# Optimization experiments

Hardware: AMD Instinct MI355X
Metric: run time of the kernel (lower is better)

Reference implementation:

```python
import jax, jax.numpy as jnp
import numpy as np

N_HEADS = 16
D_MODEL = 1024
D_K = D_MODEL // N_HEADS
B, S = 2, 2048


def setup_inputs() -> dict:
    key = jax.random.key(0)
    ks = jax.random.split(key, 12)
    sc = 1.0 / np.sqrt(D_MODEL)
    inp = {
        'query': jax.random.normal(ks[0], (B, S, D_MODEL), jnp.float32),
        'key':   jax.random.normal(ks[1], (B, S, D_MODEL), jnp.float32),
        'value': jax.random.normal(ks[2], (B, S, D_MODEL), jnp.float32),
        'mask':  jnp.ones((B, 1, 1, S), jnp.int32),
        'Wq': jax.random.normal(ks[3], (D_MODEL, D_MODEL), jnp.float32) * sc,
        'bq': jnp.zeros((D_MODEL,), jnp.float32),
        'Wk': jax.random.normal(ks[4], (D_MODEL, D_MODEL), jnp.float32) * sc,
        'bk': jnp.zeros((D_MODEL,), jnp.float32),
        'Wv': jax.random.normal(ks[5], (D_MODEL, D_MODEL), jnp.float32) * sc,
        'bv': jnp.zeros((D_MODEL,), jnp.float32),
        'Wo': jax.random.normal(ks[6], (D_MODEL, D_MODEL), jnp.float32) * sc,
        'bo': jnp.zeros((D_MODEL,), jnp.float32),
    }
    return inp


def reference(query, key, value, mask, Wq, bq, Wk, bk, Wv, bv, Wo, bo):
    # Linear projections (torch Linear: x @ W.T + b)
    q = query @ Wq.T + bq
    k = key @ Wk.T + bk
    v = value @ Wv.T + bv
    # [B, S, D] -> [B, H, S, d_k]
    def split_heads(x):
        b, s, _ = x.shape
        return x.reshape(b, s, N_HEADS, D_K).transpose(0, 2, 1, 3)
    q, k, v = split_heads(q), split_heads(k), split_heads(v)
    # scaled dot-product attention with explicit [B,H,S,S] scores
    att = jnp.einsum('bhqd,bhkd->bhqk', q, k) / jnp.sqrt(jnp.float32(D_K))
    att = jnp.where(mask == 0, -jnp.inf, att)
    scores = jax.nn.softmax(att, axis=-1)
    # dropout is identity in eval/reference mode
    out = jnp.einsum('bhqk,bhkd->bhqd', scores, v)
    b = out.shape[0]
    out = out.transpose(0, 2, 1, 3).reshape(b, -1, N_HEADS * D_K)
    return out @ Wo.T + bo
```

## Files before the change

kernel.cpp:

```cpp
#include <hip/hip_runtime.h>
#include <hip/hip_bf16.h>

#define DM   1024
#define SLEN 2048
#define NH   16
#define DK   64

typedef float f32x4 __attribute__((ext_vector_type(4)));
typedef short short8 __attribute__((ext_vector_type(8)));
typedef short short4v __attribute__((ext_vector_type(4)));

__device__ __forceinline__ unsigned short f2bf(float f) {
  union { float f; unsigned int u; } x; x.f = f;
  unsigned int r = x.u + 0x7fffu + ((x.u >> 16) & 1u);
  return (unsigned short)(r >> 16);
}

__device__ __forceinline__ void gload_lds16(const unsigned short* g, unsigned short* l) {
  __builtin_amdgcn_global_load_lds(
      (const __attribute__((address_space(1))) unsigned int*)g,
      (__attribute__((address_space(3))) unsigned int*)l, 16, 0, 0);
}

__device__ __forceinline__ f32x4 mfma32(short8 a, short8 b, f32x4 c) {
  return __builtin_amdgcn_mfma_f32_16x16x32_bf16(a, b, c, 0, 0, 0);
}

__device__ __forceinline__ f32x4 mfma16(short4v a, short4v b, f32x4 c) {
#if __has_builtin(__builtin_amdgcn_mfma_f32_16x16x16bf16_1k)
  return __builtin_amdgcn_mfma_f32_16x16x16bf16_1k(a, b, c, 0, 0, 0);
#else
  f32x4 d;
  asm volatile("v_mfma_f32_16x16x16_bf16 %0, %1, %2, %3"
               : "=v"(d) : "v"(a), "v"(b), "v"(c));
  return d;
#endif
}

struct ConvArgs { const float* src[7]; unsigned short* dst[7]; };

__global__ __launch_bounds__(256) void conv_kernel(ConvArgs a) {
  int blk = blockIdx.x, seg, base;
  if (blk < 6144) { seg = blk >> 11; base = blk & 2047; }
  else { int t = blk - 6144; seg = 3 + (t >> 9); base = t & 511; }
  const float* s = a.src[seg];
  unsigned short* d = a.dst[seg];
  int idx = (base * 256 + (int)threadIdx.x) * 8;
  float4 v0 = *(const float4*)(s + idx);
  float4 v1 = *(const float4*)(s + idx + 4);
  unsigned short o[8];
  o[0]=f2bf(v0.x); o[1]=f2bf(v0.y); o[2]=f2bf(v0.z); o[3]=f2bf(v0.w);
  o[4]=f2bf(v1.x); o[5]=f2bf(v1.y); o[6]=f2bf(v1.z); o[7]=f2bf(v1.w);
  *(uint4*)(d + idx) = *(uint4*)o;
}

template <int TN>
__device__ __forceinline__ void gemm_core(int mode,
                                          const unsigned short* __restrict__ A,
                                          const unsigned short* __restrict__ W,
                                          const float* __restrict__ bias,
                                          void* __restrict__ outp, float scale,
                                          int m0, int n0,
                                          unsigned short* As, unsigned short* Bs) {
  const int tid = threadIdx.x;
  const int lane = tid & 63;
  const int l15 = lane & 15;
  const int quad = lane >> 4;
  const int wv = tid >> 6;
  const int wm = (wv >> 1) * 64, wn = (wv & 1) * (TN / 2);
  const int NB = TN / 32;

  f32x4 acc[4][NB];
#pragma unroll
  for (int i = 0; i < 4; ++i)
#pragma unroll
    for (int j = 0; j < NB; ++j) acc[i][j] = (f32x4){0.f, 0.f, 0.f, 0.f};

  for (int k0 = 0; k0 < DM; k0 += 64) {
    __syncthreads();
#pragma unroll
    for (int i = 0; i < 4; ++i) {
      int c = tid + i * 256;
      int row = c >> 3, sc = ((c & 7) ^ (row & 7)) << 3;
      gload_lds16(A + (size_t)(m0 + row) * DM + k0 + sc, As + c * 8);
    }
#pragma unroll
    for (int i = 0; i < NB; ++i) {
      int c = tid + i * 256;
      int row = c >> 3, sc = ((c & 7) ^ (row & 7)) << 3;
      gload_lds16(W + (size_t)(n0 + row) * DM + k0 + sc, Bs + c * 8);
    }
    __syncthreads();
    short8 af[4][2], bf[NB][2];
#pragma unroll
    for (int i = 0; i < 4; ++i) {
      int r = wm + i * 16 + l15;
#pragma unroll
      for (int kf = 0; kf < 2; ++kf)
        af[i][kf] = *(const short8*)(As + r * 64 + (((kf * 4 + quad) ^ (r & 7)) << 3));
    }
#pragma unroll
    for (int j = 0; j < NB; ++j) {
      int r = wn + j * 16 + l15;
#pragma unroll
      for (int kf = 0; kf < 2; ++kf)
        bf[j][kf] = *(const short8*)(Bs + r * 64 + (((kf * 4 + quad) ^ (r & 7)) << 3));
    }
#pragma unroll
    for (int kf = 0; kf < 2; ++kf)
#pragma unroll
      for (int i = 0; i < 4; ++i)
#pragma unroll
        for (int j = 0; j < NB; ++j)
          acc[i][j] = mfma32(af[i][kf], bf[j][kf], acc[i][j]);
  }

#pragma unroll
  for (int i = 0; i < 4; ++i)
#pragma unroll
    for (int j = 0; j < NB; ++j) {
      int col = n0 + wn + j * 16 + l15;
      float bv = bias[col];
      int row0 = wm + i * 16 + (quad << 2) + m0;
      if (mode == 2) {
        unsigned short pk[4];
#pragma unroll
        for (int g = 0; g < 4; ++g) pk[g] = f2bf(acc[i][j][g] + bv);
        int d = col & (DK - 1), hh = col >> 6;
        int brow = row0 >> 11, srow = row0 & (SLEN - 1);
        size_t idx = ((size_t)((brow * NH + hh) * DK + d)) * SLEN + srow;
        *(uint2*)(((unsigned short*)outp) + idx) = *(uint2*)pk;
      } else if (mode == 0) {
#pragma unroll
        for (int g = 0; g < 4; ++g) {
          int row = row0 + g;
          float v = (acc[i][j][g] + bv) * scale;
          size_t idx = ((size_t)((row >> 11) * NH + (col >> 6))) * (SLEN * DK) +
                       (size_t)(row & (SLEN - 1)) * DK + (col & (DK - 1));
          ((unsigned short*)outp)[idx] = f2bf(v);
        }
      } else {
#pragma unroll
        for (int g = 0; g < 4; ++g)
          ((float*)outp)[(size_t)(row0 + g) * DM + col] = acc[i][j][g] + bv;
      }
    }
}

struct QKVArgs {
  const unsigned short* A[3];
  const unsigned short* W[3];
  const float* bias[3];
  unsigned short* out[3];
  float scale[3];
  int mode[3];
};

__global__ __launch_bounds__(256) void gemm_qkv_kernel(QKVArgs a) {
  __shared__ unsigned short As[128 * 64], Bs[128 * 64];
  int z = blockIdx.z;
  gemm_core<128>(a.mode[z], a.A[z], a.W[z], a.bias[z], a.out[z], a.scale[z],
                 blockIdx.x * 128, blockIdx.y * 128, As, Bs);
}

__global__ __launch_bounds__(256) void gemm_o_kernel(const unsigned short* __restrict__ A,
                                                     const unsigned short* __restrict__ W,
                                                     const float* __restrict__ bias,
                                                     float* __restrict__ out) {
  __shared__ unsigned short As[128 * 64], Bs[64 * 64];
  gemm_core<64>(1, A, W, bias, out, 1.0f, blockIdx.x * 128, blockIdx.y * 64, As, Bs);
}

__global__ __launch_bounds__(512, 4) void attn_kernel(
    const unsigned short* __restrict__ Qw,
    const unsigned short* __restrict__ Kw,
    const unsigned short* __restrict__ Vtw,
    const int* __restrict__ mask,
    unsigned short* __restrict__ attn_out) {
  __shared__ uint4 smem4[3264];
  char* smb = (char*)smem4;
  unsigned short* Qs = (unsigned short*)smb;

  const int tid = threadIdx.x;
  const int lane = tid & 63;
  const int l15 = lane & 15;
  const int quad = lane >> 4;
  const int wv = tid >> 6;
  const int grp = wv >> 2;
  const int widx = wv & 3;
  const int tg = tid & 255;

  unsigned short* KstG = (unsigned short*)(smb + 18432 + grp * 8192);
  unsigned short* VstG = (unsigned short*)(smb + 34816 + grp * 8192);
  float* maskG = (float*)(smb + 51200 + grp * 256);
  float* Oex = (float*)(smb + 18432);
  float* lsX = (float*)(smb + 51456);

  const int s0 = blockIdx.x * 128;
  const int bh = blockIdx.y;
  const int b = bh >> 4, h = bh & 15;
  const unsigned short* Qb = Qw + (size_t)bh * (SLEN * DK);
  const unsigned short* Kb = Kw + (size_t)bh * (SLEN * DK);
  const unsigned short* Vtb = Vtw + (size_t)bh * (SLEN * DK);

#pragma unroll
  for (int i = 0; i < 2; ++i) {
    int seg = tid + i * 512;
    int row = seg >> 3, d0 = (seg & 7) << 3;
    *(uint4*)(Qs + row * 72 + d0) = *(const uint4*)(Qb + (size_t)(s0 + row) * DK + d0);
  }

  const int c0 = tg, c1 = tg + 256;
  const int r0c = c0 >> 3, s0c = ((c0 & 7) ^ (r0c & 7)) << 3;
  const int r1c = c1 >> 3, s1c = ((c1 & 7) ^ (r1c & 7)) << 3;

  int kv0 = grp * 64;
  gload_lds16(Kb + (size_t)(kv0 + r0c) * DK + s0c, KstG + c0 * 8);
  gload_lds16(Kb + (size_t)(kv0 + r1c) * DK + s1c, KstG + c1 * 8);
  gload_lds16(Vtb + (size_t)r0c * SLEN + kv0 + s0c, VstG + c0 * 8);
  gload_lds16(Vtb + (size_t)r1c * SLEN + kv0 + s1c, VstG + c1 * 8);
  int mreg = (tg < 64) ? mask[b * SLEN + kv0 + tg] : 1;
  __syncthreads();
  if (tg < 64) {
    maskG[tg] = mreg ? 0.0f : -1e30f;
    mreg = mask[b * SLEN + (2 + grp) * 64 + tg];
  }
  __syncthreads();

  const int qb = widx * 32;
  short8 bq[2][2];
#pragma unroll
  for (int qt = 0; qt < 2; ++qt)
#pragma unroll
    for (int kf = 0; kf < 2; ++kf)
      bq[qt][kf] = *(const short8*)(Qs + (qb + qt * 16 + l15) * 72 + kf * 32 + quad * 8);

  f32x4 O[4][2];
#pragma unroll
  for (int dt = 0; dt < 4; ++dt)
#pragma unroll
    for (int qt = 0; qt < 2; ++qt) O[dt][qt] = (f32x4){0.f, 0.f, 0.f, 0.f};
  float lsum[2] = {0.f, 0.f};

  for (int it = 0; it < 16; ++it) {
    f32x4 st[4][2];
#pragma unroll
    for (int ct = 0; ct < 4; ++ct) {
      int r = ct * 16 + l15;
      short8 ka0 = *(const short8*)(KstG + r * 64 + ((quad ^ (r & 7)) << 3));
      short8 ka1 = *(const short8*)(KstG + r * 64 + (((4 + quad) ^ (r & 7)) << 3));
#pragma unroll
      for (int qt = 0; qt < 2; ++qt) {
        f32x4 z = (f32x4){0.f, 0.f, 0.f, 0.f};
        z = mfma32(ka0, bq[qt][0], z);
        st[ct][qt] = mfma32(ka1, bq[qt][1], z);
      }
    }
    short4v pf[4][2];
#pragma unroll
    for (int ct = 0; ct < 4; ++ct) {
      f32x4 ma = *(const f32x4*)(maskG + ct * 16 + quad * 4);
#pragma unroll
      for (int qt = 0; qt < 2; ++qt) {
        float p0 = __builtin_exp2f(st[ct][qt][0] + ma[0]);
        float p1 = __builtin_exp2f(st[ct][qt][1] + ma[1]);
        float p2 = __builtin_exp2f(st[ct][qt][2] + ma[2]);
        float p3 = __builtin_exp2f(st[ct][qt][3] + ma[3]);
        lsum[qt] += (p0 + p1) + (p2 + p3);
        union { short4v s; __hip_bfloat162 h[2]; } u;
        u.h[0] = __float22bfloat162_rn(float2{p0, p1});
        u.h[1] = __float22bfloat162_rn(float2{p2, p3});
        pf[ct][qt] = u.s;
      }
    }
#pragma unroll
    for (int dt = 0; dt < 4; ++dt) {
      int rd = dt * 16 + l15;
      short4v vf[4];
#pragma unroll
      for (int ct = 0; ct < 4; ++ct) {
        int slot = (ct * 2 + (quad >> 1)) ^ (rd & 7);
        vf[ct] = *(const short4v*)(VstG + rd * 64 + slot * 8 + (quad & 1) * 4);
      }
#pragma unroll
      for (int qt = 0; qt < 2; ++qt)
#pragma unroll
        for (int ct = 0; ct < 4; ++ct)
          O[dt][qt] = mfma16(vf[ct], pf[ct][qt], O[dt][qt]);
    }
    __syncthreads();
    if (it < 15) {
      int kvn = ((it + 1) * 2 + grp) * 64;
      gload_lds16(Kb + (size_t)(kvn + r0c) * DK + s0c, KstG + c0 * 8);
      gload_lds16(Kb + (size_t)(kvn + r1c) * DK + s1c, KstG + c1 * 8);
      gload_lds16(Vtb + (size_t)r0c * SLEN + kvn + s0c, VstG + c0 * 8);
      gload_lds16(Vtb + (size_t)r1c * SLEN + kvn + s1c, VstG + c1 * 8);
      if (tg < 64) {
        maskG[tg] = mreg ? 0.0f : -1e30f;
        if (it < 14) mreg = mask[b * SLEN + ((it + 2) * 2 + grp) * 64 + tg];
      }
      __syncthreads();
    }
  }

#pragma unroll
  for (int qt = 0; qt < 2; ++qt) {
    lsum[qt] += __shfl_xor(lsum[qt], 16);
    lsum[qt] += __shfl_xor(lsum[qt], 32);
  }
  if (grp == 1) {
#pragma unroll
    for (int dt = 0; dt < 4; ++dt)
#pragma unroll
      for (int qt = 0; qt < 2; ++qt) {
        int qg = qb + qt * 16 + l15;
#pragma unroll
        for (int i = 0; i < 4; ++i)
          Oex[(dt * 16 + quad * 4 + i) * 129 + qg] = O[dt][qt][i];
      }
    if (quad == 0) {
      lsX[qb + lane] = lsum[0];
      lsX[qb + 16 + lane] = lsum[1];
    }
  }
  __syncthreads();
  if (grp == 0) {
#pragma unroll
    for (int qt = 0; qt < 2; ++qt) {
      int qg = qb + qt * 16 + l15;
      float inv = 1.0f / (lsum[qt] + lsX[qg]);
      int srow = s0 + qg;
#pragma unroll
      for (int dt = 0; dt < 4; ++dt) {
        int d0 = dt * 16 + quad * 4;
        unsigned short pk[4];
#pragma unroll
        for (int i = 0; i < 4; ++i)
          pk[i] = f2bf((O[dt][qt][i] + Oex[(d0 + i) * 129 + qg]) * inv);
        *(uint2*)(attn_out + (size_t)(b * SLEN + srow) * DM + h * DK + d0) = *(uint2*)pk;
      }
    }
  }
}

extern "C" void kernel_launch(void* const* d_in, const int* in_sizes, int n_in,
                              void* d_out, int out_size, void* d_ws, size_t ws_size,
                              hipStream_t stream) {
  (void)in_sizes; (void)n_in; (void)out_size; (void)ws_size;
  const float* query = (const float*)d_in[0];
  const float* key_  = (const float*)d_in[1];
  const float* value = (const float*)d_in[2];
  const int*   mask  = (const int*)d_in[3];
  const float* Wq = (const float*)d_in[4];
  const float* bq = (const float*)d_in[5];
  const float* Wk = (const float*)d_in[6];
  const float* bk = (const float*)d_in[7];
  const float* Wv = (const float*)d_in[8];
  const float* bv = (const float*)d_in[9];
  const float* Wo = (const float*)d_in[10];
  const float* bo = (const float*)d_in[11];
  float* out = (float*)d_out;

  const size_t WSZ = 1048576, XSZ = 4194304;
  unsigned short* base = (unsigned short*)d_ws;
  unsigned short* Wqb = base;
  unsigned short* Wkb = base + WSZ;
  unsigned short* Wvb = base + 2 * WSZ;
  unsigned short* Wob = base + 3 * WSZ;
  unsigned short* Xqb = base + 4 * WSZ;
  unsigned short* Xkb = Xqb + XSZ;
  unsigned short* Xvb = Xqb + 2 * XSZ;
  unsigned short* Qw  = Xqb + 3 * XSZ;
  unsigned short* Kw  = Qw + XSZ;
  unsigned short* Vtw = Qw + 2 * XSZ;
  unsigned short* attnb = Qw + 3 * XSZ;

  ConvArgs ca;
  ca.src[0] = query; ca.src[1] = key_; ca.src[2] = value;
  ca.src[3] = Wq; ca.src[4] = Wk; ca.src[5] = Wv; ca.src[6] = Wo;
  ca.dst[0] = Xqb; ca.dst[1] = Xkb; ca.dst[2] = Xvb;
  ca.dst[3] = Wqb; ca.dst[4] = Wkb; ca.dst[5] = Wvb; ca.dst[6] = Wob;
  conv_kernel<<<8192, 256, 0, stream>>>(ca);

  QKVArgs qa;
  qa.A[0] = Xqb; qa.A[1] = Xkb; qa.A[2] = Xvb;
  qa.W[0] = Wqb; qa.W[1] = Wkb; qa.W[2] = Wvb;
  qa.bias[0] = bq; qa.bias[1] = bk; qa.bias[2] = bv;
  qa.out[0] = Qw; qa.out[1] = Kw; qa.out[2] = Vtw;
  qa.scale[0] = 0.18033688011112042f;
  qa.scale[1] = 1.0f; qa.scale[2] = 1.0f;
  qa.mode[0] = 0; qa.mode[1] = 0; qa.mode[2] = 2;
  gemm_qkv_kernel<<<dim3(32, 8, 3), 256, 0, stream>>>(qa);

  attn_kernel<<<dim3(16, 32), 512, 0, stream>>>(Qw, Kw, Vtw, mask, attnb);

  gemm_o_kernel<<<dim3(32, 16), 256, 0, stream>>>(attnb, Wob, bo, out);
}
```

Baseline: 248.4 us.

## Double-buffer K/V tiles in attention, load Q to registers, shrink QKV GEMM tiles

The attention kernel now double-buffers its K, V^T and mask tiles in LDS. The next tile's global-to-LDS loads are issued before computing on the current one, which removes the second barrier per iteration. Q fragments are read straight from global into registers instead of being staged through LDS. The QKV projection GEMM moves to 128x64 tiles with a doubled grid and launch-bounds occupancy hints on both GEMMs. LDS use per attention block grows to about 66KB, which could lower occupancy.

```diff
diff --git a/kernel.cpp b/kernel.cpp
--- a/kernel.cpp
+++ b/kernel.cpp
@@ -156,17 +156,17 @@
   int mode[3];
 };
 
-__global__ __launch_bounds__(256) void gemm_qkv_kernel(QKVArgs a) {
-  __shared__ unsigned short As[128 * 64], Bs[128 * 64];
+__global__ __launch_bounds__(256, 4) void gemm_qkv_kernel(QKVArgs a) {
+  __shared__ unsigned short As[128 * 64], Bs[64 * 64];
   int z = blockIdx.z;
-  gemm_core<128>(a.mode[z], a.A[z], a.W[z], a.bias[z], a.out[z], a.scale[z],
-                 blockIdx.x * 128, blockIdx.y * 128, As, Bs);
-}
-
-__global__ __launch_bounds__(256) void gemm_o_kernel(const unsigned short* __restrict__ A,
-                                                     const unsigned short* __restrict__ W,
-                                                     const float* __restrict__ bias,
-                                                     float* __restrict__ out) {
+  gemm_core<64>(a.mode[z], a.A[z], a.W[z], a.bias[z], a.out[z], a.scale[z],
+                blockIdx.x * 128, blockIdx.y * 64, As, Bs);
+}
+
+__global__ __launch_bounds__(256, 4) void gemm_o_kernel(const unsigned short* __restrict__ A,
+                                                        const unsigned short* __restrict__ W,
+                                                        const float* __restrict__ bias,
+                                                        float* __restrict__ out) {
   __shared__ unsigned short As[128 * 64], Bs[64 * 64];
   gemm_core<64>(1, A, W, bias, out, 1.0f, blockIdx.x * 128, blockIdx.y * 64, As, Bs);
 }
@@ -177,9 +177,10 @@
     const unsigned short* __restrict__ Vtw,
     const int* __restrict__ mask,
     unsigned short* __restrict__ attn_out) {
-  __shared__ uint4 smem4[3264];
+  __shared__ uint4 smem4[4160];
   char* smb = (char*)smem4;
-  unsigned short* Qs = (unsigned short*)smb;
+  float* Oex = (float*)smb;
+  float* lsX = (float*)(smb + 33024);
 
   const int tid = threadIdx.x;
   const int lane = tid & 63;
@@ -190,12 +191,6 @@
   const int widx = wv & 3;
   const int tg = tid & 255;
 
-  unsigned short* KstG = (unsigned short*)(smb + 18432 + grp * 8192);
-  unsigned short* VstG = (unsigned short*)(smb + 34816 + grp * 8192);
-  float* maskG = (float*)(smb + 51200 + grp * 256);
-  float* Oex = (float*)(smb + 18432);
-  float* lsX = (float*)(smb + 51456);
-
   const int s0 = blockIdx.x * 128;
   const int bh = blockIdx.y;
   const int b = bh >> 4, h = bh & 15;
@@ -203,37 +198,33 @@
   const unsigned short* Kb = Kw + (size_t)bh * (SLEN * DK);
   const unsigned short* Vtb = Vtw + (size_t)bh * (SLEN * DK);
 
-#pragma unroll
-  for (int i = 0; i < 2; ++i) {
-    int seg = tid + i * 512;
-    int row = seg >> 3, d0 = (seg & 7) << 3;
-    *(uint4*)(Qs + row * 72 + d0) = *(const uint4*)(Qb + (size_t)(s0 + row) * DK + d0);
-  }
+  const int qb = widx * 32;
+  short8 bq[2][2];
+#pragma unroll
+  for (int qt = 0; qt < 2; ++qt)
+#pragma unroll
+    for (int kf = 0; kf < 2; ++kf)
+      bq[qt][kf] = *(const short8*)(Qb + (size_t)(s0 + qb + qt * 16 + l15) * DK + kf * 32 + quad * 8);
 
   const int c0 = tg, c1 = tg + 256;
   const int r0c = c0 >> 3, s0c = ((c0 & 7) ^ (r0c & 7)) << 3;
   const int r1c = c1 >> 3, s1c = ((c1 & 7) ^ (r1c & 7)) << 3;
 
-  int kv0 = grp * 64;
-  gload_lds16(Kb + (size_t)(kv0 + r0c) * DK + s0c, KstG + c0 * 8);
-  gload_lds16(Kb + (size_t)(kv0 + r1c) * DK + s1c, KstG + c1 * 8);
-  gload_lds16(Vtb + (size_t)r0c * SLEN + kv0 + s0c, VstG + c0 * 8);
-  gload_lds16(Vtb + (size_t)r1c * SLEN + kv0 + s1c, VstG + c1 * 8);
-  int mreg = (tg < 64) ? mask[b * SLEN + kv0 + tg] : 1;
+  {
+    unsigned short* K0 = (unsigned short*)(smb + grp * 8192);
+    unsigned short* V0 = (unsigned short*)(smb + 32768 + grp * 8192);
+    int kv0 = grp * 64;
+    gload_lds16(Kb + (size_t)(kv0 + r0c) * DK + s0c, K0 + c0 * 8);
+    gload_lds16(Kb + (size_t)(kv0 + r1c) * DK + s1c, K0 + c1 * 8);
+    gload_lds16(Vtb + (size_t)r0c * SLEN + kv0 + s0c, V0 + c0 * 8);
+    gload_lds16(Vtb + (size_t)r1c * SLEN + kv0 + s1c, V0 + c1 * 8);
+  }
+  int mreg = 1;
+  if (tg < 64) {
+    ((float*)(smb + 65536 + grp * 256))[tg] = mask[b * SLEN + grp * 64 + tg] ? 0.0f : -1e30f;
+    mreg = mask[b * SLEN + (2 + grp) * 64 + tg];
+  }
   __syncthreads();
-  if (tg < 64) {
-    maskG[tg] = mreg ? 0.0f : -1e30f;
-    mreg = mask[b * SLEN + (2 + grp) * 64 + tg];
-  }
-  __syncthreads();
-
-  const int qb = widx * 32;
-  short8 bq[2][2];
-#pragma unroll
-  for (int qt = 0; qt < 2; ++qt)
-#pragma unroll
-    for (int kf = 0; kf < 2; ++kf)
-      bq[qt][kf] = *(const short8*)(Qs + (qb + qt * 16 + l15) * 72 + kf * 32 + quad * 8);
 
   f32x4 O[4][2];
 #pragma unroll
@@ -242,7 +233,27 @@
     for (int qt = 0; qt < 2; ++qt) O[dt][qt] = (f32x4){0.f, 0.f, 0.f, 0.f};
   float lsum[2] = {0.f, 0.f};
 
+  int cb = 0;
   for (int it = 0; it < 16; ++it) {
+    const int nb = cb ^ 1;
+    if (it < 15) {
+      unsigned short* Kn = (unsigned short*)(smb + grp * 8192 + nb * 16384);
+      unsigned short* Vn = (unsigned short*)(smb + 32768 + grp * 8192 + nb * 16384);
+      int kvn = ((it + 1) * 2 + grp) * 64;
+      gload_lds16(Kb + (size_t)(kvn + r0c) * DK + s0c, Kn + c0 * 8);
+      gload_lds16(Kb + (size_t)(kvn + r1c) * DK + s1c, Kn + c1 * 8);
+      gload_lds16(Vtb + (size_t)r0c * SLEN + kvn + s0c, Vn + c0 * 8);
+      gload_lds16(Vtb + (size_t)r1c * SLEN + kvn + s1c, Vn + c1 * 8);
+      if (tg < 64) {
+        ((float*)(smb + 65536 + nb * 512 + grp * 256))[tg] = mreg ? 0.0f : -1e30f;
+        if (it < 14) mreg = mask[b * SLEN + ((it + 2) * 2 + grp) * 64 + tg];
+      }
+    }
+
+    unsigned short* KstG = (unsigned short*)(smb + grp * 8192 + cb * 16384);
+    unsigned short* VstG = (unsigned short*)(smb + 32768 + grp * 8192 + cb * 16384);
+    float* maskG = (float*)(smb + 65536 + cb * 512 + grp * 256);
+
     f32x4 st[4][2];
 #pragma unroll
     for (int ct = 0; ct < 4; ++ct) {
@@ -289,18 +300,7 @@
           O[dt][qt] = mfma16(vf[ct], pf[ct][qt], O[dt][qt]);
     }
     __syncthreads();
-    if (it < 15) {
-      int kvn = ((it + 1) * 2 + grp) * 64;
-      gload_lds16(Kb + (size_t)(kvn + r0c) * DK + s0c, KstG + c0 * 8);
-      gload_lds16(Kb + (size_t)(kvn + r1c) * DK + s1c, KstG + c1 * 8);
-      gload_lds16(Vtb + (size_t)r0c * SLEN + kvn + s0c, VstG + c0 * 8);
-      gload_lds16(Vtb + (size_t)r1c * SLEN + kvn + s1c, VstG + c1 * 8);
-      if (tg < 64) {
-        maskG[tg] = mreg ? 0.0f : -1e30f;
-        if (it < 14) mreg = mask[b * SLEN + ((it + 2) * 2 + grp) * 64 + tg];
-      }
-      __syncthreads();
-    }
+    cb = nb;
   }
 
 #pragma unroll
@@ -390,7 +390,7 @@
   qa.scale[0] = 0.18033688011112042f;
   qa.scale[1] = 1.0f; qa.scale[2] = 1.0f;
   qa.mode[0] = 0; qa.mode[1] = 0; qa.mode[2] = 2;
-  gemm_qkv_kernel<<<dim3(32, 8, 3), 256, 0, stream>>>(qa);
+  gemm_qkv_kernel<<<dim3(32, 16, 3), 256, 0, stream>>>(qa);
 
   attn_kernel<<<dim3(16, 32), 512, 0, stream>>>(Qw, Kw, Vtw, mask, attnb);
 
```

After: 249.9 us. About the same (+0.6%).
